# Kernel tuning notes

Hardware: AMD Instinct MI355X
Metric: run time of the kernel (lower is better)

## Reference

```python
import jax, jax.numpy as jnp
import numpy as np

E = 256
NH = 8
HD = E // NH
N, L, H, W = 8, 300, 96, 96


def setup_inputs() -> dict:
    key = jax.random.key(0)
    ks = jax.random.split(key, 9)
    s = 0.02
    return {
        "query_row": jax.random.normal(ks[0], (N, L, E), jnp.float32),
        "query_col": jax.random.normal(ks[1], (N, L, E), jnp.float32),
        "key_row": jax.random.normal(ks[2], (N, H, W, E), jnp.float32),
        "key_col": jax.random.normal(ks[3], (N, H, W, E), jnp.float32),
        "value": jax.random.normal(ks[4], (N, H, W, E), jnp.float32),
        "in_proj_weight": jax.random.normal(ks[5], (5 * E, E), jnp.float32) * s,
        "in_proj_bias": jax.random.normal(ks[6], (5 * E,), jnp.float32) * s,
        "out_proj_weight": jax.random.normal(ks[7], (E, E), jnp.float32) * s,
        "out_proj_bias": jax.random.normal(ks[8], (E,), jnp.float32) * s,
    }


def reference(query_row, query_col, key_row, key_col, value,
              in_proj_weight, in_proj_bias, out_proj_weight, out_proj_bias):
    n, l, e = query_row.shape
    _, h, w, _ = value.shape
    scale = float(HD) ** -0.5

    def proj(x, i):
        wi = in_proj_weight[i * E:(i + 1) * E]
        bi = in_proj_bias[i * E:(i + 1) * E]
        return x @ wi.T + bi

    q_row = proj(query_row, 0) * scale              # (N,L,E)
    q_col = proj(query_col, 1) * scale              # (N,L,E)
    k_row = proj(key_row, 2).mean(axis=1)           # (N,W,E)  mean over H
    k_col = proj(key_col, 3).mean(axis=2)           # (N,H,E)  mean over W
    v = proj(value, 4)                              # (N,H,W,E)

    qr = q_row.reshape(n, l, NH, HD)
    qc = q_col.reshape(n, l, NH, HD)
    kr = k_row.reshape(n, w, NH, HD)
    kc = k_col.reshape(n, h, NH, HD)
    vh = v.reshape(n, h, w, NH, HD)

    # row/col attention scores, softmax over source axis
    a_row = jax.nn.softmax(jnp.einsum('nled,nwed->nelw', qr, kr), axis=-1)  # (N,NH,L,W)
    a_col = jax.nn.softmax(jnp.einsum('nled,nhed->nelh', qc, kc), axis=-1)  # (N,NH,L,H)

    # col-then-row contraction (original else-branch: src_len_col >= src_len_row)
    out_col = jnp.einsum('nelh,nhwed->nelwd', a_col, vh)   # (N,NH,L,W,HD)
    out = jnp.einsum('nelw,nelwd->nled', a_row, out_col)    # (N,L,NH,HD)

    attn_output = out.transpose(1, 0, 2, 3).reshape(l, n, e)  # (L,N,E)
    return attn_output @ out_proj_weight.T + out_proj_bias
```

## Files before the change

kernel.cpp:

```cpp
#include <hip/hip_runtime.h>
#include <stdint.h>

typedef unsigned short u16;
typedef unsigned int   u32;
typedef __attribute__((ext_vector_type(8))) short bf16x8;
typedef __attribute__((ext_vector_type(4))) float f32x4;

static constexpr float kScale = 0.17677669529663687f;

__device__ __forceinline__ float bfl(u32 dw){ union{u32 u; float f;} x; x.u = dw << 16;        return x.f; }
__device__ __forceinline__ float bfh(u32 dw){ union{u32 u; float f;} x; x.u = dw & 0xffff0000u; return x.f; }
__device__ __forceinline__ float bf2f(u16 v){ union{u32 u; float f;} x; x.u = ((u32)v) << 16;  return x.f; }
__device__ __forceinline__ u16  f2bf(float f){
  union{float f; u32 u;} x; x.f = f;
  u32 r = x.u + 0x7fffu + ((x.u >> 16) & 1u);
  return (u16)(r >> 16);
}

__global__ void detect_kernel(const u16* __restrict__ bias, int* __restrict__ flag){
  int tid = threadIdx.x;
  u16 raw = bias[tid * 2];
  int big = (fabsf(bf2f(raw)) > 1e6f) ? 1 : 0;
  if ((raw & 0x7F80u) == 0x7F80u) big = 1;
  #pragma unroll
  for (int m = 1; m < 64; m <<= 1) big |= __shfl_xor(big, m);
  if (tid == 0) *flag = big;
}

__global__ void means_kernel(const void* __restrict__ key_row, const void* __restrict__ key_col,
                             float* __restrict__ krm, float* __restrict__ kcm,
                             const int* __restrict__ flag){
  const bool isf32 = (*flag != 0);
  int g   = blockIdx.x * 256 + threadIdx.x;
  int c8  = (g & 31) * 8;
  int ri  = g >> 5;
  int rw  = ri % 96;
  int n   = ri / 96;
  float acc[8];
  #pragma unroll
  for (int i = 0; i < 8; i++) acc[i] = 0.f;

  size_t base, stride;
  const void* src;
  float* dst;
  if (blockIdx.y == 0){
    src    = key_row;
    base   = ((size_t)(n*96)*96 + rw)*256 + c8;
    stride = (size_t)96*256;
    dst    = krm + ((size_t)(n*96) + rw)*256 + c8;
  } else {
    src    = key_col;
    base   = ((size_t)(n*96) + rw)*(size_t)(96*256) + c8;
    stride = 256;
    dst    = kcm + ((size_t)(n*96) + rw)*256 + c8;
  }

  if (isf32){
    const float* p = (const float*)src + base;
    for (int t = 0; t < 96; t++){
      float4 f0 = *(const float4*)(p + t*stride);
      float4 f1 = *(const float4*)(p + t*stride + 4);
      acc[0]+=f0.x; acc[1]+=f0.y; acc[2]+=f0.z; acc[3]+=f0.w;
      acc[4]+=f1.x; acc[5]+=f1.y; acc[6]+=f1.z; acc[7]+=f1.w;
    }
  } else {
    const u16* p = (const u16*)src + base;
    for (int t = 0; t < 96; t++){
      uint4 u = *(const uint4*)(p + t*stride);
      acc[0]+=bfl(u.x); acc[1]+=bfh(u.x); acc[2]+=bfl(u.y); acc[3]+=bfh(u.y);
      acc[4]+=bfl(u.z); acc[5]+=bfh(u.z); acc[6]+=bfl(u.w); acc[7]+=bfh(u.w);
    }
  }
  #pragma unroll
  for (int i = 0; i < 8; i++) dst[i] = acc[i] * (1.f/96.f);
}

template<int XK, int OBF, int OMAP>
__global__ __launch_bounds__(256) void mfma_proj_kernel(
    const void* __restrict__ Xv,
    const void* __restrict__ Wv, int wslice,
    const void* __restrict__ Bv, int boff,
    void* __restrict__ Yv,
    int M, float scale, int head0, int hg,
    const int* __restrict__ flag){
  const bool isf32 = (*flag != 0);
  const bool xf32  = (XK == 0) || isf32;
  __shared__ __align__(16) u16 Xs[64*40];
  __shared__ __align__(16) u16 Ws[64*40];
  __shared__ u16 stile[64*66];

  int tid = threadIdx.x;
  int m0  = blockIdx.x * 64;
  int j0  = blockIdx.y * 64;
  int wv  = tid >> 6;
  int ln  = tid & 63;
  int l15 = ln & 15;
  int quad = ln >> 4;
  int mh  = wv & 1;
  int nh  = wv >> 1;

  int srow = tid >> 2;
  int sko  = (tid & 3) * 8;

  f32x4 acc[2][2] = {{{0.f,0.f,0.f,0.f},{0.f,0.f,0.f,0.f}},
                     {{0.f,0.f,0.f,0.f},{0.f,0.f,0.f,0.f}}};

  int gm = m0 + srow;
  int wrow = j0 + srow;
  if (OMAP == 3){ wrow += head0*32; if (wrow > 255) wrow = 255; }

  for (int p = 0; p < 8; p++){
    int k0 = p * 32;
    u16 xl[8], wl[8];
    if (gm < M){
      size_t xoff = (size_t)gm*256 + k0 + sko;
      if (xf32){
        const float* xp = (const float*)Xv + xoff;
        float4 f0 = *(const float4*)xp;
        float4 f1 = *(const float4*)(xp + 4);
        xl[0]=f2bf(f0.x); xl[1]=f2bf(f0.y); xl[2]=f2bf(f0.z); xl[3]=f2bf(f0.w);
        xl[4]=f2bf(f1.x); xl[5]=f2bf(f1.y); xl[6]=f2bf(f1.z); xl[7]=f2bf(f1.w);
      } else {
        *(uint4*)xl = *(const uint4*)((const u16*)Xv + xoff);
      }
    } else {
      #pragma unroll
      for (int i = 0; i < 8; i++) xl[i] = 0;
    }
    {
      size_t woff = (size_t)wslice*65536 + (size_t)wrow*256 + k0 + sko;
      if (isf32){
        const float* wp = (const float*)Wv + woff;
        float4 f0 = *(const float4*)wp;
        float4 f1 = *(const float4*)(wp + 4);
        wl[0]=f2bf(f0.x); wl[1]=f2bf(f0.y); wl[2]=f2bf(f0.z); wl[3]=f2bf(f0.w);
        wl[4]=f2bf(f1.x); wl[5]=f2bf(f1.y); wl[6]=f2bf(f1.z); wl[7]=f2bf(f1.w);
      } else {
        *(uint4*)wl = *(const uint4*)((const u16*)Wv + woff);
      }
    }
    __syncthreads();
    *(uint4*)(Xs + srow*40 + sko) = *(uint4*)xl;
    *(uint4*)(Ws + srow*40 + sko) = *(uint4*)wl;
    __syncthreads();

    bf16x8 a0 = *(const bf16x8*)(Xs + (mh*32 +      l15)*40 + quad*8);
    bf16x8 a1 = *(const bf16x8*)(Xs + (mh*32 + 16 + l15)*40 + quad*8);
    bf16x8 b0 = *(const bf16x8*)(Ws + (nh*32 +      l15)*40 + quad*8);
    bf16x8 b1 = *(const bf16x8*)(Ws + (nh*32 + 16 + l15)*40 + quad*8);
    acc[0][0] = __builtin_amdgcn_mfma_f32_16x16x32_bf16(a0, b0, acc[0][0], 0,0,0);
    acc[0][1] = __builtin_amdgcn_mfma_f32_16x16x32_bf16(a0, b1, acc[0][1], 0,0,0);
    acc[1][0] = __builtin_amdgcn_mfma_f32_16x16x32_bf16(a1, b0, acc[1][0], 0,0,0);
    acc[1][1] = __builtin_amdgcn_mfma_f32_16x16x32_bf16(a1, b1, acc[1][1], 0,0,0);
  }

  float bv[2];
  #pragma unroll
  for (int tj = 0; tj < 2; tj++){
    int bidx = j0 + nh*32 + tj*16 + l15;
    if (OMAP == 3 && bidx > hg*32 - 1) bidx = hg*32 - 1;
    bv[tj] = isf32 ? ((const float*)Bv)[boff + bidx] : bf2f(((const u16*)Bv)[boff + bidx]);
  }

  if (OMAP == 3){
    __syncthreads();
    #pragma unroll
    for (int ti = 0; ti < 2; ti++)
      #pragma unroll
      for (int tj = 0; tj < 2; tj++)
        #pragma unroll
        for (int reg = 0; reg < 4; reg++)
          stile[(mh*32 + ti*16 + quad*4 + reg)*66 + nh*32 + tj*16 + l15] =
              f2bf(scale * (acc[ti][tj][reg] + bv[tj]));
    __syncthreads();
    int hw_i = tid & 63;
    int m    = m0 + hw_i;
    int nn   = m / 9216;
    int hwin = m - nn*9216;
    int hh   = hwin / 96, ww = hwin - hh*96;
    #pragma unroll
    for (int e = 0; e < 16; e++){
      int d_col = (tid >> 6) * 16 + e;
      int col   = j0 + d_col;
      if (col < hg*32){
        int gsv = nn*hg + (col >> 5), d = col & 31;
        ((u16*)Yv)[ (((size_t)gsv*96 + hh)*32 + d)*96 + ww ] = stile[hw_i*66 + d_col];
      }
    }
    return;
  }

  #pragma unroll
  for (int ti = 0; ti < 2; ti++)
    #pragma unroll
    for (int tj = 0; tj < 2; tj++)
      #pragma unroll
      for (int reg = 0; reg < 4; reg++){
        int m = m0 + mh*32 + ti*16 + quad*4 + reg;
        if (m >= M) continue;
        int col = j0 + nh*32 + tj*16 + l15;
        float vval = scale * (acc[ti][tj][reg] + bv[tj]);
        int orow = (OMAP == 1) ? ((m % 300)*8 + (m / 300)) : m;
        size_t oidx = (size_t)orow*256 + col;
        if (OBF == 2){
          if (isf32) ((float*)Yv)[oidx] = vval; else ((u16*)Yv)[oidx] = f2bf(vval);
        } else if (OBF == 1) ((u16*)Yv)[oidx] = f2bf(vval);
        else                 ((float*)Yv)[oidx] = vval;
      }
}

__global__ __launch_bounds__(64) void attn_weights_kernel(
    const u16* __restrict__ qr, const float* __restrict__ kr,
    const u16* __restrict__ qc, const float* __restrict__ kc,
    u16* __restrict__ arow, u16* __restrict__ acol,
    int head0, int hg){
  __shared__ float qs[30*32];
  int lt = blockIdx.x;
  int gs = blockIdx.y;
  int n  = gs / hg;
  int head = head0 + (gs % hg);
  const u16*   q = blockIdx.z ? qc : qr;
  const float* k = blockIdx.z ? kc : kr;
  u16*         a = blockIdx.z ? acol : arow;
  int lane = threadIdx.x;
  int l0   = lt * 30;

  for (int i = lane; i < 960; i += 64){
    int li = i >> 5, d = i & 31;
    qs[i] = bf2f(q[((size_t)(n*300) + l0 + li)*256 + head*32 + d]);
  }

  bool has2 = (lane < 32);
  float k1[32], k2[32];
  {
    const float* kp = k + ((size_t)(n*96) + lane)*256 + head*32;
    #pragma unroll
    for (int d4 = 0; d4 < 8; d4++){
      float4 f = *(const float4*)(kp + d4*4);
      k1[d4*4+0]=f.x; k1[d4*4+1]=f.y; k1[d4*4+2]=f.z; k1[d4*4+3]=f.w;
    }
    int w2c = has2 ? (64 + lane) : 95;
    const float* kp2 = k + ((size_t)(n*96) + w2c)*256 + head*32;
    #pragma unroll
    for (int d4 = 0; d4 < 8; d4++){
      float4 f = *(const float4*)(kp2 + d4*4);
      k2[d4*4+0]=f.x; k2[d4*4+1]=f.y; k2[d4*4+2]=f.z; k2[d4*4+3]=f.w;
    }
  }
  __syncthreads();

  for (int li = 0; li < 30; li++){
    const float* qv = qs + li*32;
    float s1 = 0.f, s2 = 0.f;
    #pragma unroll
    for (int d4 = 0; d4 < 8; d4++){
      float4 f = *(const float4*)(qv + d4*4);
      s1 += f.x*k1[d4*4+0] + f.y*k1[d4*4+1] + f.z*k1[d4*4+2] + f.w*k1[d4*4+3];
      s2 += f.x*k2[d4*4+0] + f.y*k2[d4*4+1] + f.z*k2[d4*4+2] + f.w*k2[d4*4+3];
    }
    float m = fmaxf(s1, has2 ? s2 : -1e30f);
    #pragma unroll
    for (int mask = 1; mask < 64; mask <<= 1) m = fmaxf(m, __shfl_xor(m, mask));
    float e1 = __expf(s1 - m);
    float e2 = has2 ? __expf(s2 - m) : 0.f;
    float s  = e1 + e2;
    #pragma unroll
    for (int mask = 1; mask < 64; mask <<= 1) s += __shfl_xor(s, mask);
    float inv = 1.f / s;
    u16* dst = a + ((size_t)gs*300 + l0 + li)*96;
    dst[lane] = f2bf(e1 * inv);
    if (has2) dst[64 + lane] = f2bf(e2 * inv);
  }
}

__global__ __launch_bounds__(256) void rcda_core_kernel(
    const u16* __restrict__ arow, const u16* __restrict__ acol,
    const u16* __restrict__ v, float* __restrict__ attn, int head0, int hg){
  __shared__ __align__(16) u16 vt[4*32*104];
  __shared__ __align__(16) u16 aw[32*96];
  __shared__ float cs[32*97];
  __shared__ float red[2*64*8];

  int b   = blockIdx.x;
  int xcd = b & 7;
  int jj  = b >> 3;
  int lt  = jj % 10;
  int gg  = jj / 10;
  int gs  = gg*8 + xcd;
  int n   = gs / hg;
  int head = head0 + (gs % hg);
  int l0  = lt * 32;
  int tid = threadIdx.x;
  int wv  = tid >> 6;
  int ln  = tid & 63;
  int l15 = ln & 15;
  int quad = ln >> 4;
  int nt  = wv & 1;
  int hp  = wv >> 1;

  for (int i = tid; i < 384; i += 256){
    int row = i / 12, rem = i - row*12;
    int lc = l0 + row; if (lc > 299) lc = 299;
    *(uint4*)(aw + row*96 + rem*8) = *(const uint4*)(arow + ((size_t)gs*300 + lc)*96 + rem*8);
  }
  for (int i = tid; i < 3072; i += 256){
    int row = i / 96, col = i - row*96;
    int lc = l0 + row; if (lc > 299) lc = 299;
    cs[row*97 + col] = bf2f(acol[((size_t)gs*300 + lc)*96 + col]);
  }
  __syncthreads();

  bf16x8 afr[2][3];
  #pragma unroll
  for (int mt = 0; mt < 2; mt++)
    #pragma unroll
    for (int ks = 0; ks < 3; ks++)
      afr[mt][ks] = *(const bf16x8*)(aw + (mt*16 + l15)*96 + ks*32 + quad*8);

  f32x4 out[2] = {{0.f,0.f,0.f,0.f},{0.f,0.f,0.f,0.f}};
  const u16* vbase = v + (size_t)gs * 96*32*96;

  for (int cc = 0; cc < 24; cc++){
    __syncthreads();
    const uint4* gsrc = (const uint4*)(vbase + (size_t)cc * 4*32*96);
    #pragma unroll
    for (int it = 0; it < 6; it++){
      int i = tid + it*256;
      int row = i / 12, rem = i - row*12;
      *(uint4*)((char*)vt + row*208 + rem*16) = gsrc[i];
    }
    __syncthreads();

    #pragma unroll
    for (int hh = 0; hh < 2; hh++){
      int h = hp*2 + hh;
      bf16x8 bfr[3];
      #pragma unroll
      for (int ks = 0; ks < 3; ks++)
        bfr[ks] = *(const bf16x8*)(vt + (h*32 + nt*16 + l15)*104 + ks*32 + quad*8);
      int habs = cc*4 + h;
      #pragma unroll
      for (int mt = 0; mt < 2; mt++){
        f32x4 t = {0.f,0.f,0.f,0.f};
        t = __builtin_amdgcn_mfma_f32_16x16x32_bf16(afr[mt][0], bfr[0], t, 0,0,0);
        t = __builtin_amdgcn_mfma_f32_16x16x32_bf16(afr[mt][1], bfr[1], t, 0,0,0);
        t = __builtin_amdgcn_mfma_f32_16x16x32_bf16(afr[mt][2], bfr[2], t, 0,0,0);
        #pragma unroll
        for (int reg = 0; reg < 4; reg++){
          float sc = cs[(mt*16 + quad*4 + reg)*97 + habs];
          out[mt][reg] += sc * t[reg];
        }
      }
    }
  }

  __syncthreads();
  if (hp == 1){
    float* r = red + ((size_t)(nt*64 + ln))*8;
    #pragma unroll
    for (int mt = 0; mt < 2; mt++)
      #pragma unroll
      for (int reg = 0; reg < 4; reg++) r[mt*4 + reg] = out[mt][reg];
  }
  __syncthreads();
  if (hp == 0){
    const float* r = red + ((size_t)(nt*64 + ln))*8;
    #pragma unroll
    for (int mt = 0; mt < 2; mt++){
      #pragma unroll
      for (int reg = 0; reg < 4; reg++){
        int l = l0 + mt*16 + quad*4 + reg;
        if (l < 300)
          attn[((size_t)(n*300) + l)*256 + head*32 + nt*16 + l15] = out[mt][reg] + r[mt*4 + reg];
      }
    }
  }
}

extern "C" void kernel_launch(void* const* d_in, const int* in_sizes, int n_in,
                              void* d_out, int out_size, void* d_ws, size_t ws_size,
                              hipStream_t stream){
  const void* query_row = d_in[0];
  const void* query_col = d_in[1];
  const void* key_row   = d_in[2];
  const void* key_col   = d_in[3];
  const void* value     = d_in[4];
  const void* in_w      = d_in[5];
  const void* in_b      = d_in[6];
  const void* out_w     = d_in[7];
  const void* out_b     = d_in[8];

  int hg = 1;
  {
    const size_t fixed = 8061184, per = 5640192;
    if      (ws_size >= fixed + 8*per) hg = 8;
    else if (ws_size >= fixed + 4*per) hg = 4;
    else if (ws_size >= fixed + 2*per) hg = 2;
    else                               hg = 1;
  }

  char* ws = (char*)d_ws;
  int*  flag = (int*)ws;
  size_t SV = (size_t)hg * 8 * 9216 * 32 * 2;
  size_t SA = (size_t)hg * 8 * 300 * 96 * 2;
  size_t off = 256;
  u16*   v_slab = (u16*)(ws + off); off += SV;
  u16*   arow   = (u16*)(ws + off); off += SA;
  u16*   acol   = (u16*)(ws + off); off += SA;
  u16*   qr     = (u16*)(ws + off); off += 1228800;
  u16*   qc     = (u16*)(ws + off); off += 1228800;
  float* krm    = (float*)(ws + off); off += 786432;
  float* kcm    = (float*)(ws + off); off += 786432;
  float* kr     = (float*)(ws + off); off += 786432;
  float* kc     = (float*)(ws + off); off += 786432;
  float* attn   = (float*)(ws + off); off += 2457600;

  detect_kernel<<<1, 64, 0, stream>>>((const u16*)in_b, flag);

  means_kernel<<<dim3(96, 2), 256, 0, stream>>>(key_row, key_col, krm, kcm, flag);

  mfma_proj_kernel<2,1,0><<<dim3(38, 4), 256, 0, stream>>>(query_row, in_w, 0, in_b, 0,   qr, 2400, kScale, 0, hg, flag);
  mfma_proj_kernel<2,1,0><<<dim3(38, 4), 256, 0, stream>>>(query_col, in_w, 1, in_b, 256, qc, 2400, kScale, 0, hg, flag);
  mfma_proj_kernel<0,0,0><<<dim3(12, 4), 256, 0, stream>>>(krm,       in_w, 2, in_b, 512, kr, 768,  1.f,    0, hg, flag);
  mfma_proj_kernel<0,0,0><<<dim3(12, 4), 256, 0, stream>>>(kcm,       in_w, 3, in_b, 768, kc, 768,  1.f,    0, hg, flag);

  for (int head0 = 0; head0 < 8; head0 += hg){
    int gy = (hg*32 + 63) / 64;
    mfma_proj_kernel<2,1,3><<<dim3(1152, gy), 256, 0, stream>>>(
        value, in_w, 4, in_b, 1024 + head0*32, v_slab, 73728, 1.f, head0, hg, flag);
    attn_weights_kernel<<<dim3(10, 8*hg, 2), 64, 0, stream>>>(qr, kr, qc, kc, arow, acol, head0, hg);
    rcda_core_kernel<<<dim3(10 * 8 * hg), 256, 0, stream>>>(arow, acol, v_slab, attn, head0, hg);
  }

  mfma_proj_kernel<0,2,1><<<dim3(38, 4), 256, 0, stream>>>(attn, out_w, 0, out_b, 0, d_out, 2400, 1.f, 0, hg, flag);
}
```

Measured before the change: 404.9 us.

## Pre-convert weights to bf16 and restructure projection GEMM with full-K X tile

Adds a prep kernel that converts all in/out projection weights to bf16 once. The projection kernel is rewritten to stage a full 64x256 X tile in LDS, read B fragments straight from the bf16 weights, and have each block cover up to 256 output columns (NJ tiles), so X is loaded and converted only once. The q_row/q_col and key projections are merged into one launch each, and the attention output becomes a bf16 intermediate to halve its traffic. The cost is fewer blocks per launch, a larger LDS footprint and extra bf16 rounding of the attention output.

```diff
diff --git a/kernel.cpp b/kernel.cpp
--- a/kernel.cpp
+++ b/kernel.cpp
@@ -25,6 +25,29 @@
   #pragma unroll
   for (int m = 1; m < 64; m <<= 1) big |= __shfl_xor(big, m);
   if (tid == 0) *flag = big;
+}
+
+__global__ __launch_bounds__(256) void prep_weights_kernel(
+    const void* __restrict__ in_w, const void* __restrict__ out_w,
+    u16* __restrict__ Wbf, const int* __restrict__ flag){
+  const bool isf32 = (*flag != 0);
+  int idx = blockIdx.x * 256 + threadIdx.x;
+  size_t off = (size_t)idx * 8;
+  const size_t IN_ELEMS = (size_t)1280 * 256;
+  bool isout = off >= IN_ELEMS;
+  const void* src = isout ? out_w : in_w;
+  size_t soff = isout ? off - IN_ELEMS : off;
+  u16 xl[8];
+  if (isf32){
+    const float* p = (const float*)src + soff;
+    float4 f0 = *(const float4*)p;
+    float4 f1 = *(const float4*)(p + 4);
+    xl[0]=f2bf(f0.x); xl[1]=f2bf(f0.y); xl[2]=f2bf(f0.z); xl[3]=f2bf(f0.w);
+    xl[4]=f2bf(f1.x); xl[5]=f2bf(f1.y); xl[6]=f2bf(f1.z); xl[7]=f2bf(f1.w);
+  } else {
+    *(uint4*)xl = *(const uint4*)((const u16*)src + soff);
+  }
+  *(uint4*)(Wbf + off) = *(uint4*)xl;
 }
 
 __global__ void means_kernel(const void* __restrict__ key_row, const void* __restrict__ key_col,
@@ -75,138 +98,151 @@
   for (int i = 0; i < 8; i++) dst[i] = acc[i] * (1.f/96.f);
 }
 
-template<int XK, int OBF, int OMAP>
-__global__ __launch_bounds__(256) void mfma_proj_kernel(
-    const void* __restrict__ Xv,
-    const void* __restrict__ Wv, int wslice,
-    const void* __restrict__ Bv, int boff,
-    void* __restrict__ Yv,
+template<int XF, int OBF, int OMAP, int NJ>
+__global__ __launch_bounds__(256) void mfma_proj2(
+    const void* __restrict__ Xv0, const void* __restrict__ Xv1,
+    const u16* __restrict__ Wbf, int wr00, int wr01,
+    const void* __restrict__ Bv, int bo0, int bo1,
+    void* __restrict__ Yv0, void* __restrict__ Yv1,
     int M, float scale, int head0, int hg,
     const int* __restrict__ flag){
   const bool isf32 = (*flag != 0);
-  const bool xf32  = (XK == 0) || isf32;
-  __shared__ __align__(16) u16 Xs[64*40];
-  __shared__ __align__(16) u16 Ws[64*40];
-  __shared__ u16 stile[64*66];
-
-  int tid = threadIdx.x;
-  int m0  = blockIdx.x * 64;
-  int j0  = blockIdx.y * 64;
-  int wv  = tid >> 6;
-  int ln  = tid & 63;
-  int l15 = ln & 15;
-  int quad = ln >> 4;
-  int mh  = wv & 1;
-  int nh  = wv >> 1;
-
-  int srow = tid >> 2;
-  int sko  = (tid & 3) * 8;
-
-  f32x4 acc[2][2] = {{{0.f,0.f,0.f,0.f},{0.f,0.f,0.f,0.f}},
-                     {{0.f,0.f,0.f,0.f},{0.f,0.f,0.f,0.f}}};
-
-  int gm = m0 + srow;
-  int wrow = j0 + srow;
-  if (OMAP == 3){ wrow += head0*32; if (wrow > 255) wrow = 255; }
-
+  const bool xf32  = (XF == 0) || (XF == 2 && isf32);
+  __shared__ __align__(16) u16 Xs[64*264];
+  __shared__ __align__(16) u16 stile[(OMAP==3) ? 64*66 : 64];
+
+  const void* Xv  = blockIdx.y ? Xv1 : Xv0;
+  const int wrow0 = blockIdx.y ? wr01 : wr00;
+  const int boff  = blockIdx.y ? bo1  : bo0;
+  void* Yv        = blockIdx.y ? Yv1 : Yv0;
+
+  const int tid = threadIdx.x;
+  const int m0  = blockIdx.x * 64;
+  const int wv  = tid >> 6, ln = tid & 63;
+  const int l15 = ln & 15, quad = ln >> 4;
+  const int mh  = wv & 1,  nh = wv >> 1;
+
+  {
+    const int srow = tid >> 2;
+    const int sko  = (tid & 3) * 8;
+    const int gm   = m0 + srow;
+    #pragma unroll
+    for (int c = 0; c < 8; c++){
+      const int k = c*32 + sko;
+      u16 xl[8];
+      if (gm < M){
+        const size_t xoff = (size_t)gm*256 + k;
+        if (xf32){
+          const float* xp = (const float*)Xv + xoff;
+          float4 f0 = *(const float4*)xp;
+          float4 f1 = *(const float4*)(xp + 4);
+          xl[0]=f2bf(f0.x); xl[1]=f2bf(f0.y); xl[2]=f2bf(f0.z); xl[3]=f2bf(f0.w);
+          xl[4]=f2bf(f1.x); xl[5]=f2bf(f1.y); xl[6]=f2bf(f1.z); xl[7]=f2bf(f1.w);
+        } else {
+          *(uint4*)xl = *(const uint4*)((const u16*)Xv + xoff);
+        }
+      } else {
+        #pragma unroll
+        for (int i = 0; i < 8; i++) xl[i] = 0;
+      }
+      *(uint4*)(Xs + srow*264 + k) = *(uint4*)xl;
+    }
+  }
+  __syncthreads();
+
+  f32x4 acc[NJ][2][2];
+  #pragma unroll
+  for (int jt = 0; jt < NJ; jt++)
+    #pragma unroll
+    for (int i = 0; i < 2; i++)
+      #pragma unroll
+      for (int j = 0; j < 2; j++)
+        acc[jt][i][j] = (f32x4){0.f,0.f,0.f,0.f};
+
+  const int rmax = (OMAP == 3) ? (1279 - wrow0) : 1535;
+
+  #pragma unroll
   for (int p = 0; p < 8; p++){
-    int k0 = p * 32;
-    u16 xl[8], wl[8];
-    if (gm < M){
-      size_t xoff = (size_t)gm*256 + k0 + sko;
-      if (xf32){
-        const float* xp = (const float*)Xv + xoff;
-        float4 f0 = *(const float4*)xp;
-        float4 f1 = *(const float4*)(xp + 4);
-        xl[0]=f2bf(f0.x); xl[1]=f2bf(f0.y); xl[2]=f2bf(f0.z); xl[3]=f2bf(f0.w);
-        xl[4]=f2bf(f1.x); xl[5]=f2bf(f1.y); xl[6]=f2bf(f1.z); xl[7]=f2bf(f1.w);
-      } else {
-        *(uint4*)xl = *(const uint4*)((const u16*)Xv + xoff);
+    const int k0 = p * 32;
+    bf16x8 a0 = *(const bf16x8*)(Xs + (mh*32      + l15)*264 + k0 + quad*8);
+    bf16x8 a1 = *(const bf16x8*)(Xs + (mh*32 + 16 + l15)*264 + k0 + quad*8);
+    #pragma unroll
+    for (int jt = 0; jt < NJ; jt++){
+      int r0 = jt*64 + nh*32      + l15; if (r0 > rmax) r0 = rmax;
+      int r1 = jt*64 + nh*32 + 16 + l15; if (r1 > rmax) r1 = rmax;
+      bf16x8 b0 = *(const bf16x8*)(Wbf + (size_t)(wrow0 + r0)*256 + k0 + quad*8);
+      bf16x8 b1 = *(const bf16x8*)(Wbf + (size_t)(wrow0 + r1)*256 + k0 + quad*8);
+      acc[jt][0][0] = __builtin_amdgcn_mfma_f32_16x16x32_bf16(a0, b0, acc[jt][0][0], 0,0,0);
+      acc[jt][0][1] = __builtin_amdgcn_mfma_f32_16x16x32_bf16(a0, b1, acc[jt][0][1], 0,0,0);
+      acc[jt][1][0] = __builtin_amdgcn_mfma_f32_16x16x32_bf16(a1, b0, acc[jt][1][0], 0,0,0);
+      acc[jt][1][1] = __builtin_amdgcn_mfma_f32_16x16x32_bf16(a1, b1, acc[jt][1][1], 0,0,0);
+    }
+  }
+
+  if (OMAP == 3){
+    const int hw_i = tid & 63;
+    const int mg   = m0 + hw_i;
+    const int nn   = mg / 9216;
+    const int hwin = mg - nn*9216;
+    const int hh   = hwin / 96, ww = hwin - hh*96;
+    #pragma unroll
+    for (int jt = 0; jt < NJ; jt++){
+      float bvv[2];
+      #pragma unroll
+      for (int tj = 0; tj < 2; tj++){
+        int bidx = jt*64 + nh*32 + tj*16 + l15;
+        if (bidx > hg*32 - 1) bidx = hg*32 - 1;
+        bvv[tj] = isf32 ? ((const float*)Bv)[boff + bidx] : bf2f(((const u16*)Bv)[boff + bidx]);
       }
-    } else {
-      #pragma unroll
-      for (int i = 0; i < 8; i++) xl[i] = 0;
-    }
-    {
-      size_t woff = (size_t)wslice*65536 + (size_t)wrow*256 + k0 + sko;
-      if (isf32){
-        const float* wp = (const float*)Wv + woff;
-        float4 f0 = *(const float4*)wp;
-        float4 f1 = *(const float4*)(wp + 4);
-        wl[0]=f2bf(f0.x); wl[1]=f2bf(f0.y); wl[2]=f2bf(f0.z); wl[3]=f2bf(f0.w);
-        wl[4]=f2bf(f1.x); wl[5]=f2bf(f1.y); wl[6]=f2bf(f1.z); wl[7]=f2bf(f1.w);
-      } else {
-        *(uint4*)wl = *(const uint4*)((const u16*)Wv + woff);
+      __syncthreads();
+      #pragma unroll
+      for (int ti = 0; ti < 2; ti++)
+        #pragma unroll
+        for (int tj = 0; tj < 2; tj++)
+          #pragma unroll
+          for (int reg = 0; reg < 4; reg++)
+            stile[(mh*32 + ti*16 + quad*4 + reg)*66 + nh*32 + tj*16 + l15] =
+                f2bf(scale * (acc[jt][ti][tj][reg] + bvv[tj]));
+      __syncthreads();
+      #pragma unroll
+      for (int e = 0; e < 16; e++){
+        int d_col = wv*16 + e;
+        int col   = jt*64 + d_col;
+        if (col < hg*32){
+          int gsv = nn*hg + (col >> 5), d = col & 31;
+          ((u16*)Yv)[ (((size_t)gsv*96 + hh)*32 + d)*96 + ww ] = stile[hw_i*66 + d_col];
+        }
       }
     }
-    __syncthreads();
-    *(uint4*)(Xs + srow*40 + sko) = *(uint4*)xl;
-    *(uint4*)(Ws + srow*40 + sko) = *(uint4*)wl;
-    __syncthreads();
-
-    bf16x8 a0 = *(const bf16x8*)(Xs + (mh*32 +      l15)*40 + quad*8);
-    bf16x8 a1 = *(const bf16x8*)(Xs + (mh*32 + 16 + l15)*40 + quad*8);
-    bf16x8 b0 = *(const bf16x8*)(Ws + (nh*32 +      l15)*40 + quad*8);
-    bf16x8 b1 = *(const bf16x8*)(Ws + (nh*32 + 16 + l15)*40 + quad*8);
-    acc[0][0] = __builtin_amdgcn_mfma_f32_16x16x32_bf16(a0, b0, acc[0][0], 0,0,0);
-    acc[0][1] = __builtin_amdgcn_mfma_f32_16x16x32_bf16(a0, b1, acc[0][1], 0,0,0);
-    acc[1][0] = __builtin_amdgcn_mfma_f32_16x16x32_bf16(a1, b0, acc[1][0], 0,0,0);
-    acc[1][1] = __builtin_amdgcn_mfma_f32_16x16x32_bf16(a1, b1, acc[1][1], 0,0,0);
-  }
-
-  float bv[2];
-  #pragma unroll
-  for (int tj = 0; tj < 2; tj++){
-    int bidx = j0 + nh*32 + tj*16 + l15;
-    if (OMAP == 3 && bidx > hg*32 - 1) bidx = hg*32 - 1;
-    bv[tj] = isf32 ? ((const float*)Bv)[boff + bidx] : bf2f(((const u16*)Bv)[boff + bidx]);
-  }
-
-  if (OMAP == 3){
-    __syncthreads();
+    return;
+  }
+
+  #pragma unroll
+  for (int jt = 0; jt < NJ; jt++){
+    float bvv[2];
+    #pragma unroll
+    for (int tj = 0; tj < 2; tj++){
+      int bidx = jt*64 + nh*32 + tj*16 + l15;
+      bvv[tj] = isf32 ? ((const float*)Bv)[boff + bidx] : bf2f(((const u16*)Bv)[boff + bidx]);
+    }
     #pragma unroll
     for (int ti = 0; ti < 2; ti++)
       #pragma unroll
       for (int tj = 0; tj < 2; tj++)
         #pragma unroll
-        for (int reg = 0; reg < 4; reg++)
-          stile[(mh*32 + ti*16 + quad*4 + reg)*66 + nh*32 + tj*16 + l15] =
-              f2bf(scale * (acc[ti][tj][reg] + bv[tj]));
-    __syncthreads();
-    int hw_i = tid & 63;
-    int m    = m0 + hw_i;
-    int nn   = m / 9216;
-    int hwin = m - nn*9216;
-    int hh   = hwin / 96, ww = hwin - hh*96;
-    #pragma unroll
-    for (int e = 0; e < 16; e++){
-      int d_col = (tid >> 6) * 16 + e;
-      int col   = j0 + d_col;
-      if (col < hg*32){
-        int gsv = nn*hg + (col >> 5), d = col & 31;
-        ((u16*)Yv)[ (((size_t)gsv*96 + hh)*32 + d)*96 + ww ] = stile[hw_i*66 + d_col];
-      }
-    }
-    return;
-  }
-
-  #pragma unroll
-  for (int ti = 0; ti < 2; ti++)
-    #pragma unroll
-    for (int tj = 0; tj < 2; tj++)
-      #pragma unroll
-      for (int reg = 0; reg < 4; reg++){
-        int m = m0 + mh*32 + ti*16 + quad*4 + reg;
-        if (m >= M) continue;
-        int col = j0 + nh*32 + tj*16 + l15;
-        float vval = scale * (acc[ti][tj][reg] + bv[tj]);
-        int orow = (OMAP == 1) ? ((m % 300)*8 + (m / 300)) : m;
-        size_t oidx = (size_t)orow*256 + col;
-        if (OBF == 2){
-          if (isf32) ((float*)Yv)[oidx] = vval; else ((u16*)Yv)[oidx] = f2bf(vval);
-        } else if (OBF == 1) ((u16*)Yv)[oidx] = f2bf(vval);
-        else                 ((float*)Yv)[oidx] = vval;
-      }
+        for (int reg = 0; reg < 4; reg++){
+          int m = m0 + mh*32 + ti*16 + quad*4 + reg;
+          if (m >= M) continue;
+          int col = jt*64 + nh*32 + tj*16 + l15;
+          float vval = scale * (acc[jt][ti][tj][reg] + bvv[tj]);
+          int orow = (OMAP == 1) ? ((m % 300)*8 + (m / 300)) : m;
+          size_t oidx = (size_t)orow*256 + col;
+          if (OBF == 2){
+            if (isf32) ((float*)Yv)[oidx] = vval; else ((u16*)Yv)[oidx] = f2bf(vval);
+          } else if (OBF == 1) ((u16*)Yv)[oidx] = f2bf(vval);
+          else                 ((float*)Yv)[oidx] = vval;
+        }
+  }
 }
 
 __global__ __launch_bounds__(64) void attn_weights_kernel(
@@ -275,7 +311,7 @@
 
 __global__ __launch_bounds__(256) void rcda_core_kernel(
     const u16* __restrict__ arow, const u16* __restrict__ acol,
-    const u16* __restrict__ v, float* __restrict__ attn, int head0, int hg){
+    const u16* __restrict__ v, u16* __restrict__ attn, int head0, int hg){
   __shared__ __align__(16) u16 vt[4*32*104];
   __shared__ __align__(16) u16 aw[32*96];
   __shared__ float cs[32*97];
@@ -371,7 +407,8 @@
       for (int reg = 0; reg < 4; reg++){
         int l = l0 + mt*16 + quad*4 + reg;
         if (l < 300)
-          attn[((size_t)(n*300) + l)*256 + head*32 + nt*16 + l15] = out[mt][reg] + r[mt*4 + reg];
+          attn[((size_t)(n*300) + l)*256 + head*32 + nt*16 + l15] =
+              f2bf(out[mt][reg] + r[mt*4 + reg]);
       }
     }
   }
@@ -392,7 +429,7 @@
 
   int hg = 1;
   {
-    const size_t fixed = 8061184, per = 5640192;
+    const size_t fixed = 7618816, per = 5640192;
     if      (ws_size >= fixed + 8*per) hg = 8;
     else if (ws_size >= fixed + 4*per) hg = 4;
     else if (ws_size >= fixed + 2*per) hg = 2;
@@ -407,30 +444,48 @@
   u16*   v_slab = (u16*)(ws + off); off += SV;
   u16*   arow   = (u16*)(ws + off); off += SA;
   u16*   acol   = (u16*)(ws + off); off += SA;
+  u16*   Wbf    = (u16*)(ws + off); off += 786432;
   u16*   qr     = (u16*)(ws + off); off += 1228800;
   u16*   qc     = (u16*)(ws + off); off += 1228800;
   float* krm    = (float*)(ws + off); off += 786432;
   float* kcm    = (float*)(ws + off); off += 786432;
   float* kr     = (float*)(ws + off); off += 786432;
   float* kc     = (float*)(ws + off); off += 786432;
-  float* attn   = (float*)(ws + off); off += 2457600;
+  u16*   attnb  = (u16*)(ws + off); off += 1228800;
 
   detect_kernel<<<1, 64, 0, stream>>>((const u16*)in_b, flag);
 
+  prep_weights_kernel<<<192, 256, 0, stream>>>(in_w, out_w, Wbf, flag);
+
   means_kernel<<<dim3(96, 2), 256, 0, stream>>>(key_row, key_col, krm, kcm, flag);
 
-  mfma_proj_kernel<2,1,0><<<dim3(38, 4), 256, 0, stream>>>(query_row, in_w, 0, in_b, 0,   qr, 2400, kScale, 0, hg, flag);
-  mfma_proj_kernel<2,1,0><<<dim3(38, 4), 256, 0, stream>>>(query_col, in_w, 1, in_b, 256, qc, 2400, kScale, 0, hg, flag);
-  mfma_proj_kernel<0,0,0><<<dim3(12, 4), 256, 0, stream>>>(krm,       in_w, 2, in_b, 512, kr, 768,  1.f,    0, hg, flag);
-  mfma_proj_kernel<0,0,0><<<dim3(12, 4), 256, 0, stream>>>(kcm,       in_w, 3, in_b, 768, kc, 768,  1.f,    0, hg, flag);
+  mfma_proj2<2,1,0,4><<<dim3(38, 2), 256, 0, stream>>>(
+      query_row, query_col, Wbf, 0, 256, in_b, 0, 256, qr, qc,
+      2400, kScale, 0, hg, flag);
+
+  mfma_proj2<0,0,0,4><<<dim3(12, 2), 256, 0, stream>>>(
+      krm, kcm, Wbf, 512, 768, in_b, 512, 768, kr, kc,
+      768, 1.f, 0, hg, flag);
 
   for (int head0 = 0; head0 < 8; head0 += hg){
-    int gy = (hg*32 + 63) / 64;
-    mfma_proj_kernel<2,1,3><<<dim3(1152, gy), 256, 0, stream>>>(
-        value, in_w, 4, in_b, 1024 + head0*32, v_slab, 73728, 1.f, head0, hg, flag);
+    int wr0 = 1024 + head0*32;
+    if (hg == 8)
+      mfma_proj2<2,1,3,4><<<dim3(1152, 1), 256, 0, stream>>>(
+          value, value, Wbf, wr0, wr0, in_b, wr0, wr0, v_slab, v_slab,
+          73728, 1.f, head0, hg, flag);
+    else if (hg == 4)
+      mfma_proj2<2,1,3,2><<<dim3(1152, 1), 256, 0, stream>>>(
+          value, value, Wbf, wr0, wr0, in_b, wr0, wr0, v_slab, v_slab,
+          73728, 1.f, head0, hg, flag);
+    else
+      mfma_proj2<2,1,3,1><<<dim3(1152, 1), 256, 0, stream>>>(
+          value, value, Wbf, wr0, wr0, in_b, wr0, wr0, v_slab, v_slab,
+          73728, 1.f, head0, hg, flag);
     attn_weights_kernel<<<dim3(10, 8*hg, 2), 64, 0, stream>>>(qr, kr, qc, kc, arow, acol, head0, hg);
-    rcda_core_kernel<<<dim3(10 * 8 * hg), 256, 0, stream>>>(arow, acol, v_slab, attn, head0, hg);
-  }
-
-  mfma_proj_kernel<0,2,1><<<dim3(38, 4), 256, 0, stream>>>(attn, out_w, 0, out_b, 0, d_out, 2400, 1.f, 0, hg, flag);
-}
+    rcda_core_kernel<<<dim3(10 * 8 * hg), 256, 0, stream>>>(arow, acol, v_slab, attnb, head0, hg);
+  }
+
+  mfma_proj2<1,2,1,4><<<dim3(38, 1), 256, 0, stream>>>(
+      attnb, attnb, Wbf, 1280, 1280, out_b, 0, 0, d_out, d_out,
+      2400, 1.f, 0, hg, flag);
+}
```

New measurement: 439.6 us. 1.09x slower.

## Pre-convert weights to bf16 once, batch paired projections, store attention output as bf16

Applied to the files above, without the earlier changes.

Adds a prep kernel that converts the in- and out-projection weights to bf16 once into a workspace buffer, so the projection kernels load bf16 weights directly instead of converting fp32 in every tile. The q_row/q_col and k_row/k_col projections are merged into single launches using blockIdx.z. The core kernel now writes its attention output in bf16, which halves that intermediate buffer and the output projection reads it as bf16. The shared staging tile is also shrunk for non-value paths. These remove redundant conversions and launches, at the cost of one extra kernel and slightly lower precision on the intermediate output.

```diff
diff --git a/kernel.cpp b/kernel.cpp
--- a/kernel.cpp
+++ b/kernel.cpp
@@ -25,6 +25,29 @@
   #pragma unroll
   for (int m = 1; m < 64; m <<= 1) big |= __shfl_xor(big, m);
   if (tid == 0) *flag = big;
+}
+
+__global__ __launch_bounds__(256) void prep_weights_kernel(
+    const void* __restrict__ in_w, const void* __restrict__ out_w,
+    u16* __restrict__ Wbf, const int* __restrict__ flag){
+  const bool isf32 = (*flag != 0);
+  int idx = blockIdx.x * 256 + threadIdx.x;
+  size_t off = (size_t)idx * 8;
+  const size_t IN_ELEMS = (size_t)1280 * 256;
+  bool isout = off >= IN_ELEMS;
+  const void* src = isout ? out_w : in_w;
+  size_t soff = isout ? off - IN_ELEMS : off;
+  u16 xl[8];
+  if (isf32){
+    const float* p = (const float*)src + soff;
+    float4 f0 = *(const float4*)p;
+    float4 f1 = *(const float4*)(p + 4);
+    xl[0]=f2bf(f0.x); xl[1]=f2bf(f0.y); xl[2]=f2bf(f0.z); xl[3]=f2bf(f0.w);
+    xl[4]=f2bf(f1.x); xl[5]=f2bf(f1.y); xl[6]=f2bf(f1.z); xl[7]=f2bf(f1.w);
+  } else {
+    *(uint4*)xl = *(const uint4*)((const u16*)src + soff);
+  }
+  *(uint4*)(Wbf + off) = *(uint4*)xl;
 }
 
 __global__ void means_kernel(const void* __restrict__ key_row, const void* __restrict__ key_col,
@@ -75,19 +98,24 @@
   for (int i = 0; i < 8; i++) dst[i] = acc[i] * (1.f/96.f);
 }
 
-template<int XK, int OBF, int OMAP>
-__global__ __launch_bounds__(256) void mfma_proj_kernel(
-    const void* __restrict__ Xv,
-    const void* __restrict__ Wv, int wslice,
-    const void* __restrict__ Bv, int boff,
-    void* __restrict__ Yv,
+template<int XF, int OBF, int OMAP>
+__global__ __launch_bounds__(256) void mfma_proj3(
+    const void* __restrict__ Xv0, const void* __restrict__ Xv1,
+    const u16* __restrict__ Wbf, int wr00, int wr01,
+    const void* __restrict__ Bv, int bo0, int bo1,
+    void* __restrict__ Yv0, void* __restrict__ Yv1,
     int M, float scale, int head0, int hg,
     const int* __restrict__ flag){
   const bool isf32 = (*flag != 0);
-  const bool xf32  = (XK == 0) || isf32;
+  const bool xf32  = (XF == 0) || (XF == 2 && isf32);
   __shared__ __align__(16) u16 Xs[64*40];
   __shared__ __align__(16) u16 Ws[64*40];
-  __shared__ u16 stile[64*66];
+  __shared__ __align__(16) u16 stile[(OMAP==3) ? 64*66 : 64];
+
+  const void* Xv  = blockIdx.z ? Xv1 : Xv0;
+  const int wrow0 = blockIdx.z ? wr01 : wr00;
+  const int boff  = blockIdx.z ? bo1  : bo0;
+  void* Yv        = blockIdx.z ? Yv1 : Yv0;
 
   int tid = threadIdx.x;
   int m0  = blockIdx.x * 64;
@@ -106,12 +134,13 @@
                      {{0.f,0.f,0.f,0.f},{0.f,0.f,0.f,0.f}}};
 
   int gm = m0 + srow;
-  int wrow = j0 + srow;
-  if (OMAP == 3){ wrow += head0*32; if (wrow > 255) wrow = 255; }
+  int wrel = j0 + srow;
+  if (OMAP == 3){ wrel += head0*32; if (wrel > 255) wrel = 255; }
+  const u16* wsrc = Wbf + (size_t)(wrow0 + wrel)*256 + sko;
 
   for (int p = 0; p < 8; p++){
     int k0 = p * 32;
-    u16 xl[8], wl[8];
+    u16 xl[8];
     if (gm < M){
       size_t xoff = (size_t)gm*256 + k0 + sko;
       if (xf32){
@@ -127,21 +156,10 @@
       #pragma unroll
       for (int i = 0; i < 8; i++) xl[i] = 0;
     }
-    {
-      size_t woff = (size_t)wslice*65536 + (size_t)wrow*256 + k0 + sko;
-      if (isf32){
-        const float* wp = (const float*)Wv + woff;
-        float4 f0 = *(const float4*)wp;
-        float4 f1 = *(const float4*)(wp + 4);
-        wl[0]=f2bf(f0.x); wl[1]=f2bf(f0.y); wl[2]=f2bf(f0.z); wl[3]=f2bf(f0.w);
-        wl[4]=f2bf(f1.x); wl[5]=f2bf(f1.y); wl[6]=f2bf(f1.z); wl[7]=f2bf(f1.w);
-      } else {
-        *(uint4*)wl = *(const uint4*)((const u16*)Wv + woff);
-      }
-    }
+    uint4 wl = *(const uint4*)(wsrc + k0);
     __syncthreads();
     *(uint4*)(Xs + srow*40 + sko) = *(uint4*)xl;
-    *(uint4*)(Ws + srow*40 + sko) = *(uint4*)wl;
+    *(uint4*)(Ws + srow*40 + sko) = wl;
     __syncthreads();
 
     bf16x8 a0 = *(const bf16x8*)(Xs + (mh*32 +      l15)*40 + quad*8);
@@ -275,7 +293,7 @@
 
 __global__ __launch_bounds__(256) void rcda_core_kernel(
     const u16* __restrict__ arow, const u16* __restrict__ acol,
-    const u16* __restrict__ v, float* __restrict__ attn, int head0, int hg){
+    const u16* __restrict__ v, u16* __restrict__ attn, int head0, int hg){
   __shared__ __align__(16) u16 vt[4*32*104];
   __shared__ __align__(16) u16 aw[32*96];
   __shared__ float cs[32*97];
@@ -371,7 +389,8 @@
       for (int reg = 0; reg < 4; reg++){
         int l = l0 + mt*16 + quad*4 + reg;
         if (l < 300)
-          attn[((size_t)(n*300) + l)*256 + head*32 + nt*16 + l15] = out[mt][reg] + r[mt*4 + reg];
+          attn[((size_t)(n*300) + l)*256 + head*32 + nt*16 + l15] =
+              f2bf(out[mt][reg] + r[mt*4 + reg]);
       }
     }
   }
@@ -392,7 +411,7 @@
 
   int hg = 1;
   {
-    const size_t fixed = 8061184, per = 5640192;
+    const size_t fixed = 7618816, per = 5640192;
     if      (ws_size >= fixed + 8*per) hg = 8;
     else if (ws_size >= fixed + 4*per) hg = 4;
     else if (ws_size >= fixed + 2*per) hg = 2;
@@ -407,30 +426,39 @@
   u16*   v_slab = (u16*)(ws + off); off += SV;
   u16*   arow   = (u16*)(ws + off); off += SA;
   u16*   acol   = (u16*)(ws + off); off += SA;
+  u16*   Wbf    = (u16*)(ws + off); off += 786432;
   u16*   qr     = (u16*)(ws + off); off += 1228800;
   u16*   qc     = (u16*)(ws + off); off += 1228800;
   float* krm    = (float*)(ws + off); off += 786432;
   float* kcm    = (float*)(ws + off); off += 786432;
   float* kr     = (float*)(ws + off); off += 786432;
   float* kc     = (float*)(ws + off); off += 786432;
-  float* attn   = (float*)(ws + off); off += 2457600;
+  u16*   attnb  = (u16*)(ws + off); off += 1228800;
 
   detect_kernel<<<1, 64, 0, stream>>>((const u16*)in_b, flag);
 
+  prep_weights_kernel<<<192, 256, 0, stream>>>(in_w, out_w, Wbf, flag);
+
   means_kernel<<<dim3(96, 2), 256, 0, stream>>>(key_row, key_col, krm, kcm, flag);
 
-  mfma_proj_kernel<2,1,0><<<dim3(38, 4), 256, 0, stream>>>(query_row, in_w, 0, in_b, 0,   qr, 2400, kScale, 0, hg, flag);
-  mfma_proj_kernel<2,1,0><<<dim3(38, 4), 256, 0, stream>>>(query_col, in_w, 1, in_b, 256, qc, 2400, kScale, 0, hg, flag);
-  mfma_proj_kernel<0,0,0><<<dim3(12, 4), 256, 0, stream>>>(krm,       in_w, 2, in_b, 512, kr, 768,  1.f,    0, hg, flag);
-  mfma_proj_kernel<0,0,0><<<dim3(12, 4), 256, 0, stream>>>(kcm,       in_w, 3, in_b, 768, kc, 768,  1.f,    0, hg, flag);
+  mfma_proj3<2,1,0><<<dim3(38, 4, 2), 256, 0, stream>>>(
+      query_row, query_col, Wbf, 0, 256, in_b, 0, 256, qr, qc,
+      2400, kScale, 0, hg, flag);
+
+  mfma_proj3<0,0,0><<<dim3(12, 4, 2), 256, 0, stream>>>(
+      krm, kcm, Wbf, 512, 768, in_b, 512, 768, kr, kc,
+      768, 1.f, 0, hg, flag);
 
   for (int head0 = 0; head0 < 8; head0 += hg){
     int gy = (hg*32 + 63) / 64;
-    mfma_proj_kernel<2,1,3><<<dim3(1152, gy), 256, 0, stream>>>(
-        value, in_w, 4, in_b, 1024 + head0*32, v_slab, 73728, 1.f, head0, hg, flag);
+    mfma_proj3<2,1,3><<<dim3(1152, gy, 1), 256, 0, stream>>>(
+        value, value, Wbf, 1024, 1024, in_b, 1024 + head0*32, 1024 + head0*32,
+        v_slab, v_slab, 73728, 1.f, head0, hg, flag);
     attn_weights_kernel<<<dim3(10, 8*hg, 2), 64, 0, stream>>>(qr, kr, qc, kc, arow, acol, head0, hg);
-    rcda_core_kernel<<<dim3(10 * 8 * hg), 256, 0, stream>>>(arow, acol, v_slab, attn, head0, hg);
-  }
-
-  mfma_proj_kernel<0,2,1><<<dim3(38, 4), 256, 0, stream>>>(attn, out_w, 0, out_b, 0, d_out, 2400, 1.f, 0, hg, flag);
-}
+    rcda_core_kernel<<<dim3(10 * 8 * hg), 256, 0, stream>>>(arow, acol, v_slab, attnb, head0, hg);
+  }
+
+  mfma_proj3<1,2,1><<<dim3(38, 4, 1), 256, 0, stream>>>(
+      attnb, attnb, Wbf, 1280, 1280, out_b, 0, 0, d_out, d_out,
+      2400, 1.f, 0, hg, flag);
+}
```

Result: faster. 365.2 us (-9.8%).
